# Kernel tuning notes

Hardware: AMD Instinct MI355X
Metric: run time of the kernel (lower is better)

## Reference

```python
import jax, jax.numpy as jnp
import numpy as np

B, S, D, H, K = 2, 2048, 1024, 16, 16


def setup_inputs() -> dict:
    key = jax.random.key(0)
    ks = jax.random.split(key, 8)
    s = 0.02
    def w(k, shape):
        return s * jax.random.normal(k, shape, jnp.float32)
    return {
        "x": jax.random.normal(ks[0], (B, S, D), jnp.float32),
        "Wq": w(ks[1], (D, D)), "bq": jnp.zeros((D,), jnp.float32),
        "Wk": w(ks[2], (D, D)), "bk": jnp.zeros((D,), jnp.float32),
        "Wv": w(ks[3], (D, D)), "bv": jnp.zeros((D,), jnp.float32),
        "Wo": w(ks[4], (D, D)), "bo": jnp.zeros((D,), jnp.float32),
        "Ws1": w(ks[5], (D, D // 2)), "bs1": jnp.zeros((D // 2,), jnp.float32),
        "Ws2": w(ks[6], (D // 2, 1)), "bs2": jnp.zeros((1,), jnp.float32),
    }


def reference(x, Wq, bq, Wk, bk, Wv, bv, Wo, bo, Ws1, bs1, Ws2, bs2):
    Bx, Sx, Dx = x.shape
    Dh = Dx // H
    # QKV projections -> [B, H, S, Dh]
    q = (x @ Wq + bq).reshape(Bx, Sx, H, Dh).transpose(0, 2, 1, 3)
    k = (x @ Wk + bk).reshape(Bx, Sx, H, Dh).transpose(0, 2, 1, 3)
    v = (x @ Wv + bv).reshape(Bx, Sx, H, Dh).transpose(0, 2, 1, 3)
    scores = jnp.einsum('bhqd,bhkd->bhqk', q, k) / np.float32(np.sqrt(Dh))
    # Lightning-indexer importance: [B, S]; identical across heads, so compute once.
    imp = jax.nn.sigmoid(jax.nn.relu(x @ Ws1 + bs1) @ Ws2 + bs2)[..., 0]
    _, idx = jax.lax.top_k(imp, K)  # [B, K]
    sel = jnp.zeros((Bx, Sx), bool).at[jnp.arange(Bx)[:, None], idx].set(True)
    # sparse mask: position (i, j) kept if row i OR column j is a top-k token
    m2 = sel[:, :, None] | sel[:, None, :]  # [B, S, S]
    masked = jnp.where(m2[:, None, :, :], scores, -jnp.inf)
    w = jax.nn.softmax(masked, axis=-1)
    att = jnp.einsum('bhqk,bhkd->bhqd', w, v).transpose(0, 2, 1, 3).reshape(Bx, Sx, Dx)
    return att @ Wo + bo
```

## Files before the change

### kernel.cpp

```cpp
#include <hip/hip_runtime.h>
#include <math.h>

constexpr int Bb = 2, Ss = 2048, Dd = 1024, Hh = 16, Kk = 16;
constexpr float DELTA = 0.02f;

typedef __bf16 bf16x8 __attribute__((ext_vector_type(8)));
typedef __bf16 bf16x4 __attribute__((ext_vector_type(4)));
typedef float  f32x4  __attribute__((ext_vector_type(4)));

__device__ __forceinline__ void gld_lds16(const void* g, void* l) {
    __builtin_amdgcn_global_load_lds(
        (const __attribute__((address_space(1))) unsigned int*)g,
        (__attribute__((address_space(3))) unsigned int*)l, 16, 0, 0);
}

__global__ void __launch_bounds__(256) prep_kernel(
    const float* __restrict__ x, __bf16* __restrict__ xb,
    __bf16* __restrict__ xbT,
    float* __restrict__ imp, float* __restrict__ hbuf,
    float* __restrict__ qkvsel, int* __restrict__ ccount,
    const float* __restrict__ Ws1, __bf16* __restrict__ W1Th,
    const float* __restrict__ bv, const float* __restrict__ bo,
    float* __restrict__ Y, float* __restrict__ zbuf,
    float* __restrict__ obuf)
{
    __shared__ float tile[32][33];
    const int bid = blockIdx.x;
    const int t   = threadIdx.x;

    if (bid < 4096) {
        int i = bid * 256 + t;
        if (i < Bb * Ss) imp[i] = 0.f;
        if (i < Bb * 64 * 512) hbuf[i] = 0.f;
        if (i < 3 * 32 * 1024) qkvsel[i] = 0.f;
        if (i < 2 * 256 * 1024) Y[i] = 0.f;
        if (i < 2 * 16 * 1024) zbuf[i] = bv[i & 1023];
        if (i < 2 * 16 * 1024) obuf[i] = bo[i & 1023];
        if (i < Bb) ccount[i] = 0;
        float4 v = ((const float4*)x)[i];
        bf16x4 h = { (__bf16)v.x, (__bf16)v.y, (__bf16)v.z, (__bf16)v.w };
        ((bf16x4*)xb)[i] = h;
        return;
    }
    if (bid < 8192) {
        int tid = bid - 4096;
        int b   = tid >> 11;
        int rem = tid & 2047;
        int rt  = rem >> 5;
        int ct  = rem & 31;
        int tx = t & 31, ty = t >> 5;
        const float* xp = x + (size_t)b * Ss * Dd;
        #pragma unroll
        for (int i2 = 0; i2 < 32; i2 += 8)
            tile[ty + i2][tx] = xp[(size_t)(rt * 32 + ty + i2) * 1024 + ct * 32 + tx];
        __syncthreads();
        __bf16* xT = xbT + (size_t)b * Dd * Ss;
        #pragma unroll
        for (int i2 = 0; i2 < 32; i2 += 8)
            xT[(size_t)(ct * 32 + ty + i2) * 2048 + rt * 32 + tx] = (__bf16)tile[tx][ty + i2];
        return;
    }
    {
        int tid = bid - 8192;
        int n0 = (tid & 15) * 32;
        int k0 = (tid >> 4) * 32;
        int tx = t & 31, ty = t >> 5;
        #pragma unroll
        for (int i2 = 0; i2 < 32; i2 += 8)
            tile[ty + i2][tx] = Ws1[(size_t)(k0 + ty + i2) * 512 + n0 + tx];
        __syncthreads();
        #pragma unroll
        for (int i2 = 0; i2 < 32; i2 += 8)
            W1Th[(size_t)(n0 + ty + i2) * 1024 + k0 + tx] = (__bf16)tile[tx][ty + i2];
    }
}

__global__ void __launch_bounds__(256) gemm_ind(
    const __bf16* __restrict__ xb, const __bf16* __restrict__ W1Th,
    const float* __restrict__ bs1, const float* __restrict__ Ws2,
    float* __restrict__ imp)
{
    __shared__ __bf16 As[64 * 64];
    __shared__ __bf16 Bs[128 * 64];

    const int cb   = blockIdx.x;
    const int bm   = blockIdx.y * 64;
    const int t    = threadIdx.x;
    const int wave = t >> 6;
    const int lane = t & 63;
    const int wm   = (wave & 1) * 32;
    const int wn   = (wave >> 1) * 64;
    const int fr   = lane & 15;
    const int fq   = lane >> 4;
    const int K    = Dd;

    const __bf16* BT = W1Th + (size_t)cb * 128 * 1024;

    f32x4 acc[2][4] = {};

    for (int k0 = 0; k0 < K; k0 += 64) {
        #pragma unroll
        for (int l = 0; l < 2; ++l) {
            int c = l * 256 + t;
            int row = c >> 3, seg = (c & 7) ^ (row & 7);
            gld_lds16(xb + (size_t)(bm + row) * K + k0 + seg * 8,
                      As + (size_t)(l * 256 + wave * 64) * 8);
        }
        #pragma unroll
        for (int l = 0; l < 4; ++l) {
            int c = l * 256 + t;
            int row = c >> 3, seg = (c & 7) ^ (row & 7);
            gld_lds16(BT + (size_t)row * K + k0 + seg * 8,
                      Bs + (size_t)(l * 256 + wave * 64) * 8);
        }
        __syncthreads();
        #pragma unroll
        for (int s = 0; s < 2; ++s) {
            bf16x8 af[2], bf[4];
            #pragma unroll
            for (int i = 0; i < 2; ++i) {
                int row = wm + i * 16 + fr;
                af[i] = *(const bf16x8*)(As + row * 64 + (((s * 4 + fq) ^ (row & 7)) * 8));
            }
            #pragma unroll
            for (int j = 0; j < 4; ++j) {
                int row = wn + j * 16 + fr;
                bf[j] = *(const bf16x8*)(Bs + row * 64 + (((s * 4 + fq) ^ (row & 7)) * 8));
            }
            #pragma unroll
            for (int i = 0; i < 2; ++i)
                #pragma unroll
                for (int j = 0; j < 4; ++j)
                    acc[i][j] = __builtin_amdgcn_mfma_f32_16x16x32_bf16(af[i], bf[j], acc[i][j], 0, 0, 0);
        }
        __syncthreads();
    }

    const int cr = (lane >> 4) * 4;
    const int cc = lane & 15;
    float bb[4], w2[4];
    #pragma unroll
    for (int j = 0; j < 4; ++j) {
        int col = cb * 128 + wn + j * 16 + cc;
        bb[j] = bs1[col];
        w2[j] = Ws2[col];
    }
    #pragma unroll
    for (int i = 0; i < 2; ++i) {
        #pragma unroll
        for (int r = 0; r < 4; ++r) {
            float vsum = 0.f;
            #pragma unroll
            for (int j = 0; j < 4; ++j)
                vsum += fmaxf(acc[i][j][r] + bb[j], 0.f) * w2[j];
            #pragma unroll
            for (int off = 8; off > 0; off >>= 1)
                vsum += __shfl_xor(vsum, off, 16);
            if (cc == 0)
                atomicAdd(imp + (bm + wm + i * 16 + cr + r), vsum);
        }
    }
}

__global__ void __launch_bounds__(1024) topk_cand(
    const float* __restrict__ imp, int* __restrict__ cand_idx,
    int* __restrict__ ccount)
{
    int b = blockIdx.x;
    int t = threadIdx.x;
    int wave = t >> 6, lane = t & 63;
    __shared__ float vals[Ss];
    __shared__ float sv[16];
    __shared__ int   si[16];
    __shared__ float thr_s;
    __shared__ int   cnt_s;

    vals[t]        = imp[b * Ss + t];
    vals[t + 1024] = imp[b * Ss + t + 1024];
    __syncthreads();

    for (int it = 0; it < Kk; ++it) {
        float v0 = vals[t], v1 = vals[t + 1024];
        float best = v0; int bidx = t;
        if (v1 > best) { best = v1; bidx = t + 1024; }
        #pragma unroll
        for (int off = 32; off > 0; off >>= 1) {
            float ov = __shfl_xor(best, off, 64);
            int   oi = __shfl_xor(bidx, off, 64);
            if (ov > best || (ov == best && oi < bidx)) { best = ov; bidx = oi; }
        }
        if (lane == 0) { sv[wave] = best; si[wave] = bidx; }
        __syncthreads();
        if (t == 0) {
            float bv = sv[0]; int br = si[0];
            #pragma unroll
            for (int w = 1; w < 16; ++w)
                if (sv[w] > bv || (sv[w] == bv && si[w] < br)) { bv = sv[w]; br = si[w]; }
            cand_idx[b * 64 + it] = br;
            vals[br] = -1e30f;
            if (it == Kk - 1) { thr_s = bv - DELTA; cnt_s = Kk; }
        }
        __syncthreads();
    }

    float thr = thr_s;
    if (vals[t] > thr) {
        int p = atomicAdd(&cnt_s, 1);
        if (p < 64) cand_idx[b * 64 + p] = t;
    }
    if (vals[t + 1024] > thr) {
        int p = atomicAdd(&cnt_s, 1);
        if (p < 64) cand_idx[b * 64 + p] = t + 1024;
    }
    __syncthreads();
    if (t == 0) ccount[b] = min(cnt_s, 64);
}

__global__ void __launch_bounds__(256) rescore_h(
    const float* __restrict__ x, const float* __restrict__ Ws1,
    const int* __restrict__ cand_idx, const int* __restrict__ ccount,
    float* __restrict__ hbuf)
{
    const int c = blockIdx.x, kc = blockIdx.y, b = blockIdx.z;
    if (c >= ccount[b]) return;
    const int row = cand_idx[b * 64 + c];
    const int t = threadIdx.x;
    const int k0 = kc * 64;

    __shared__ float xs[64];
    if (t < 16)
        ((float4*)xs)[t] = ((const float4*)(x + ((size_t)(b * Ss + row)) * Dd + k0))[t];
    __syncthreads();

    float a0 = 0.f, a1 = 0.f;
    const float* W = Ws1 + (size_t)k0 * 512;
    #pragma unroll 16
    for (int kk = 0; kk < 64; ++kk) {
        float xv = xs[kk];
        a0 = fmaf(xv, W[kk * 512 + t], a0);
        a1 = fmaf(xv, W[kk * 512 + t + 256], a1);
    }
    float* hb = hbuf + ((size_t)(b * 64 + c)) * 512;
    atomicAdd(hb + t, a0);
    atomicAdd(hb + t + 256, a1);
}

__global__ void __launch_bounds__(256) rescore_fin(
    const float* __restrict__ hbuf, const float* __restrict__ bs1,
    const float* __restrict__ Ws2, const int* __restrict__ ccount,
    float* __restrict__ candz)
{
    const int c = blockIdx.x, b = blockIdx.y;
    if (c >= ccount[b]) return;
    const int t = threadIdx.x;
    __shared__ float red[256];
    const float* hb = hbuf + ((size_t)(b * 64 + c)) * 512;
    float zp = fmaxf(hb[t] + bs1[t], 0.f) * Ws2[t]
             + fmaxf(hb[t + 256] + bs1[t + 256], 0.f) * Ws2[t + 256];
    red[t] = zp;
    __syncthreads();
    for (int off = 128; off > 0; off >>= 1) {
        if (t < off) red[t] += red[t + off];
        __syncthreads();
    }
    if (t == 0) candz[b * 64 + c] = red[0];
}

__global__ void __launch_bounds__(64) select_k(
    const float* __restrict__ candz, const int* __restrict__ cand_idx,
    const int* __restrict__ ccount, int* __restrict__ sel_idx)
{
    const int b = blockIdx.x, t = threadIdx.x;
    const int cnt = ccount[b];
    float val = (t < cnt) ? candz[b * 64 + t] : -1e30f;
    int   row = (t < cnt) ? cand_idx[b * 64 + t] : 0x7fffffff;

    for (int it = 0; it < Kk; ++it) {
        float bv = val; int br = row;
        #pragma unroll
        for (int off = 1; off < 64; off <<= 1) {
            float ov = __shfl_xor(bv, off, 64);
            int   orw = __shfl_xor(br, off, 64);
            if (ov > bv || (ov == bv && orw < br)) { bv = ov; br = orw; }
        }
        if (row == br) val = -1e30f;
        if (t == 0) sel_idx[b * Kk + it] = br;
    }
}

__global__ void __launch_bounds__(256) proj_sel(
    const float* __restrict__ x,
    const float* __restrict__ Wq, const float* __restrict__ Wk,
    const float* __restrict__ Wv,
    const int* __restrict__ sel_idx, float* __restrict__ qkvsel)
{
    const int cx = blockIdx.x;
    const int m  = blockIdx.y;
    const int kc = blockIdx.z;
    const int t  = threadIdx.x;
    __shared__ int   sj[32];
    __shared__ float xs[32][128];

    if (t < 32) sj[t] = sel_idx[t];
    __syncthreads();

    const int k0 = kc * 128;
    #pragma unroll
    for (int l = 0; l < 4; ++l) {
        int c = l * 256 + t;
        int r = c >> 5, kq = c & 31;
        int b = r >> 4;
        float4 v = *(const float4*)(x + ((size_t)(b * Ss + sj[r])) * Dd + k0 + kq * 4);
        *(float4*)&xs[r][kq * 4] = v;
    }
    __syncthreads();

    const float* W = (m == 0) ? Wq : (m == 1) ? Wk : Wv;
    const int col = cx * 128 + (t & 127);
    const int rh  = t >> 7;
    float acc[16] = {};
    #pragma unroll 4
    for (int kk = 0; kk < 128; ++kk) {
        float wv = W[(size_t)(k0 + kk) * 1024 + col];
        #pragma unroll
        for (int r = 0; r < 16; ++r)
            acc[r] = fmaf(xs[rh * 16 + r][kk], wv, acc[r]);
    }
    #pragma unroll
    for (int r = 0; r < 16; ++r)
        atomicAdd(qkvsel + (size_t)(m * 32 + rh * 16 + r) * 1024 + col, acc[r]);
}

__global__ void __launch_bounds__(256) build_cdvo(
    const float* __restrict__ Wq, const float* __restrict__ Wk,
    const float* __restrict__ Wo,
    const float* __restrict__ bq, const float* __restrict__ bk,
    const float* __restrict__ bv,
    const float* __restrict__ qkvsel, float* __restrict__ beta,
    __bf16* __restrict__ ET, __bf16* __restrict__ VoT)
{
    const int nx = blockIdx.x;
    const int h  = blockIdx.y;
    const int b  = blockIdx.z;
    const int t  = threadIdx.x;
    __shared__ float qs[16][64], ks[16][64], vs[16][64];
    __shared__ float wt[128][65];

    #pragma unroll
    for (int l = 0; l < 12; ++l) {
        int c = l * 256 + t;
        int mat = c >> 10, rem = c & 1023;
        int row = rem >> 6, d = rem & 63;
        const float* bias = (mat == 0) ? bq : (mat == 1) ? bk : bv;
        float v = qkvsel[(size_t)(mat * 32 + b * 16 + row) * 1024 + h * 64 + d]
                + bias[h * 64 + d];
        if (mat == 0) qs[row][d] = v;
        else if (mat == 1) ks[row][d] = v;
        else vs[row][d] = v;
    }
    __syncthreads();

    if (nx == 0 && t < 16) {
        float a = 0.f;
        #pragma unroll 8
        for (int d = 0; d < 64; ++d) a = fmaf(bq[h * 64 + d], ks[t][d], a);
        beta[b * 256 + h * 16 + t] = a;
    }

    const int nl = t & 127;
    const int n  = nx * 128 + nl;
    const int sg = t >> 7;

    #pragma unroll
    for (int l = 0; l < 8; ++l) {
        int c = l * 256 + t;
        int rn = c >> 4, c4 = c & 15;
        float4 v = *(const float4*)(Wq + (size_t)(nx * 128 + rn) * 1024 + h * 64 + c4 * 4);
        wt[rn][c4 * 4 + 0] = v.x; wt[rn][c4 * 4 + 1] = v.y;
        wt[rn][c4 * 4 + 2] = v.z; wt[rn][c4 * 4 + 3] = v.w;
    }
    __syncthreads();
    {
        float acc[8] = {};
        #pragma unroll 8
        for (int d = 0; d < 64; ++d) {
            float wv = wt[nl][d];
            #pragma unroll
            for (int s = 0; s < 8; ++s)
                acc[s] = fmaf(wv, ks[sg * 8 + s][d], acc[s]);
        }
        #pragma unroll
        for (int s = 0; s < 8; ++s)
            ET[(size_t)(b * 512 + h * 16 + sg * 8 + s) * 1024 + n] = (__bf16)acc[s];
    }
    __syncthreads();

    #pragma unroll
    for (int l = 0; l < 8; ++l) {
        int c = l * 256 + t;
        int rn = c >> 4, c4 = c & 15;
        float4 v = *(const float4*)(Wk + (size_t)(nx * 128 + rn) * 1024 + h * 64 + c4 * 4);
        wt[rn][c4 * 4 + 0] = v.x; wt[rn][c4 * 4 + 1] = v.y;
        wt[rn][c4 * 4 + 2] = v.z; wt[rn][c4 * 4 + 3] = v.w;
    }
    __syncthreads();
    {
        float acc[8] = {};
        #pragma unroll 8
        for (int d = 0; d < 64; ++d) {
            float wv = wt[nl][d];
            #pragma unroll
            for (int s = 0; s < 8; ++s)
                acc[s] = fmaf(wv, qs[sg * 8 + s][d], acc[s]);
        }
        #pragma unroll
        for (int s = 0; s < 8; ++s)
            ET[(size_t)(b * 512 + 256 + h * 16 + sg * 8 + s) * 1024 + n] = (__bf16)acc[s];
    }

    {
        float acc[8] = {};
        #pragma unroll 8
        for (int d = 0; d < 64; ++d) {
            float wv = Wo[(size_t)(h * 64 + d) * 1024 + n];
            #pragma unroll
            for (int s = 0; s < 8; ++s)
                acc[s] = fmaf(wv, vs[sg * 8 + s][d], acc[s]);
        }
        #pragma unroll
        for (int s = 0; s < 8; ++s)
            VoT[((size_t)b * 1024 + n) * 256 + h * 16 + sg * 8 + s] = (__bf16)acc[s];
    }
}

__global__ void __launch_bounds__(256) gemm_scores(
    const __bf16* __restrict__ xb, const __bf16* __restrict__ ET,
    float* __restrict__ Ssp, float* __restrict__ SdT)
{
    __shared__ __bf16 As[64 * 64];
    __shared__ __bf16 Bs[128 * 64];

    const int b    = blockIdx.z;
    const int bn   = blockIdx.x * 128;
    const int bm   = blockIdx.y * 64;
    const int t    = threadIdx.x;
    const int wave = t >> 6;
    const int lane = t & 63;
    const int wm   = (wave & 1) * 32;
    const int wn   = (wave >> 1) * 64;
    const int fr   = lane & 15;
    const int fq   = lane >> 4;
    const int K    = Dd;

    const __bf16* A  = xb + (size_t)b * Ss * Dd;
    const __bf16* BT = ET + (size_t)b * 512 * 1024 + (size_t)bn * 1024;

    f32x4 acc[2][4] = {};

    for (int k0 = 0; k0 < K; k0 += 64) {
        #pragma unroll
        for (int l = 0; l < 2; ++l) {
            int c = l * 256 + t;
            int row = c >> 3, seg = (c & 7) ^ (row & 7);
            gld_lds16(A + (size_t)(bm + row) * K + k0 + seg * 8,
                      As + (size_t)(l * 256 + wave * 64) * 8);
        }
        #pragma unroll
        for (int l = 0; l < 4; ++l) {
            int c = l * 256 + t;
            int row = c >> 3, seg = (c & 7) ^ (row & 7);
            gld_lds16(BT + (size_t)row * K + k0 + seg * 8,
                      Bs + (size_t)(l * 256 + wave * 64) * 8);
        }
        __syncthreads();
        #pragma unroll
        for (int s = 0; s < 2; ++s) {
            bf16x8 af[2], bf[4];
            #pragma unroll
            for (int i = 0; i < 2; ++i) {
                int row = wm + i * 16 + fr;
                af[i] = *(const bf16x8*)(As + row * 64 + (((s * 4 + fq) ^ (row & 7)) * 8));
            }
            #pragma unroll
            for (int j = 0; j < 4; ++j) {
                int row = wn + j * 16 + fr;
                bf[j] = *(const bf16x8*)(Bs + row * 64 + (((s * 4 + fq) ^ (row & 7)) * 8));
            }
            #pragma unroll
            for (int i = 0; i < 2; ++i)
                #pragma unroll
                for (int j = 0; j < 4; ++j)
                    acc[i][j] = __builtin_amdgcn_mfma_f32_16x16x32_bf16(af[i], bf[j], acc[i][j], 0, 0, 0);
        }
        __syncthreads();
    }

    const int cr = (lane >> 4) * 4;
    const int cc = lane & 15;
    #pragma unroll
    for (int j = 0; j < 4; ++j) {
        int col = bn + wn + j * 16 + cc;
        #pragma unroll
        for (int i = 0; i < 2; ++i) {
            int row0 = bm + wm + i * 16 + cr;
            if (col < 256) {
                #pragma unroll
                for (int r = 0; r < 4; ++r)
                    Ssp[((size_t)b * 2048 + row0 + r) * 256 + col] = acc[i][j][r];
            } else {
                *(f32x4*)(SdT + ((size_t)b * 256 + col - 256) * 2048 + row0) = acc[i][j];
            }
        }
    }
}

__global__ void __launch_bounds__(256) sm_sparse(
    const float* __restrict__ Ssp, const float* __restrict__ beta,
    __bf16* __restrict__ Wsp)
{
    const int b = blockIdx.y;
    const int r = blockIdx.x * 4 + (threadIdx.x >> 6);
    const int l = threadIdx.x & 63;
    float4 v  = *(const float4*)(Ssp + ((size_t)b * 2048 + r) * 256 + l * 4);
    float4 bt = *(const float4*)(beta + b * 256 + l * 4);
    float e0 = __expf((v.x + bt.x) * 0.125f);
    float e1 = __expf((v.y + bt.y) * 0.125f);
    float e2 = __expf((v.z + bt.z) * 0.125f);
    float e3 = __expf((v.w + bt.w) * 0.125f);
    float ps = e0 + e1 + e2 + e3;
    ps += __shfl_xor(ps, 1, 64);
    ps += __shfl_xor(ps, 2, 64);
    float inv = 1.f / ps;
    bf16x4 w = { (__bf16)(e0 * inv), (__bf16)(e1 * inv),
                 (__bf16)(e2 * inv), (__bf16)(e3 * inv) };
    *(bf16x4*)(Wsp + ((size_t)b * 2048 + r) * 256 + l * 4) = w;
}

__global__ void __launch_bounds__(256) sm_dense(
    const float* __restrict__ SdT, __bf16* __restrict__ WdT)
{
    const int b = blockIdx.y, cx = blockIdx.x;
    const int t = threadIdx.x;
    __shared__ float red[256];
    const float* Sp = SdT + ((size_t)b * 256 + cx) * 2048;
    float4 v0 = *(const float4*)(Sp + t * 8);
    float4 v1 = *(const float4*)(Sp + t * 8 + 4);
    float e[8];
    e[0] = __expf(v0.x * 0.125f); e[1] = __expf(v0.y * 0.125f);
    e[2] = __expf(v0.z * 0.125f); e[3] = __expf(v0.w * 0.125f);
    e[4] = __expf(v1.x * 0.125f); e[5] = __expf(v1.y * 0.125f);
    e[6] = __expf(v1.z * 0.125f); e[7] = __expf(v1.w * 0.125f);
    float ps = 0.f;
    #pragma unroll
    for (int i = 0; i < 8; ++i) ps += e[i];
    red[t] = ps;
    __syncthreads();
    for (int off = 128; off > 0; off >>= 1) {
        if (t < off) red[t] += red[t + off];
        __syncthreads();
    }
    float inv = 1.f / red[0];
    bf16x8 w;
    #pragma unroll
    for (int i = 0; i < 8; ++i) w[i] = (__bf16)(e[i] * inv);
    *(bf16x8*)(WdT + ((size_t)b * 256 + cx) * 2048 + t * 8) = w;
}

__global__ void __launch_bounds__(256) gemm_bt(
    const __bf16* __restrict__ A0, const __bf16* __restrict__ BT0,
    const float* __restrict__ bias, float* __restrict__ C0,
    int N, int K, size_t sA, size_t sB, size_t sC, int kchunks)
{
    __shared__ __bf16 As[64 * 64];
    __shared__ __bf16 Bs[128 * 64];

    const int batch = blockIdx.z / kchunks;
    const int kc    = blockIdx.z % kchunks;
    const __bf16* A  = A0 + (size_t)batch * sA;
    const __bf16* BT = BT0 + (size_t)batch * sB;
    float* C = C0 + (size_t)batch * sC;

    const int t    = threadIdx.x;
    const int wave = t >> 6;
    const int lane = t & 63;
    const int bm   = blockIdx.y * 64;
    const int bn   = blockIdx.x * 128;
    const int wm   = (wave & 1) * 32;
    const int wn   = (wave >> 1) * 64;
    const int fr   = lane & 15;
    const int fq   = lane >> 4;
    const int KC   = K / kchunks;
    const int kend = (kc + 1) * KC;

    f32x4 acc[2][4] = {};

    for (int k0 = kc * KC; k0 < kend; k0 += 64) {
        #pragma unroll
        for (int l = 0; l < 2; ++l) {
            int c = l * 256 + t;
            int row = c >> 3, seg = (c & 7) ^ (row & 7);
            gld_lds16(A + (size_t)(bm + row) * K + k0 + seg * 8,
                      As + (size_t)(l * 256 + wave * 64) * 8);
        }
        #pragma unroll
        for (int l = 0; l < 4; ++l) {
            int c = l * 256 + t;
            int row = c >> 3, seg = (c & 7) ^ (row & 7);
            gld_lds16(BT + (size_t)(bn + row) * K + k0 + seg * 8,
                      Bs + (size_t)(l * 256 + wave * 64) * 8);
        }
        __syncthreads();
        #pragma unroll
        for (int s = 0; s < 2; ++s) {
            bf16x8 af[2], bf[4];
            #pragma unroll
            for (int i = 0; i < 2; ++i) {
                int row = wm + i * 16 + fr;
                af[i] = *(const bf16x8*)(As + row * 64 + (((s * 4 + fq) ^ (row & 7)) * 8));
            }
            #pragma unroll
            for (int j = 0; j < 4; ++j) {
                int row = wn + j * 16 + fr;
                bf[j] = *(const bf16x8*)(Bs + row * 64 + (((s * 4 + fq) ^ (row & 7)) * 8));
            }
            #pragma unroll
            for (int i = 0; i < 2; ++i)
                #pragma unroll
                for (int j = 0; j < 4; ++j)
                    acc[i][j] = __builtin_amdgcn_mfma_f32_16x16x32_bf16(af[i], bf[j], acc[i][j], 0, 0, 0);
        }
        __syncthreads();
    }

    const int cr = (lane >> 4) * 4;
    const int cc = lane & 15;
    #pragma unroll
    for (int j = 0; j < 4; ++j) {
        int col = bn + wn + j * 16 + cc;
        if (kchunks == 1) {
            float bb = bias ? bias[col] : 0.f;
            #pragma unroll
            for (int i = 0; i < 2; ++i)
                #pragma unroll
                for (int r = 0; r < 4; ++r)
                    C[(size_t)(bm + wm + i * 16 + cr + r) * N + col] = acc[i][j][r] + bb;
        } else {
            #pragma unroll
            for (int i = 0; i < 2; ++i)
                #pragma unroll
                for (int r = 0; r < 4; ++r)
                    atomicAdd(C + (size_t)(bm + wm + i * 16 + cr + r) * N + col, acc[i][j][r]);
        }
    }
}

__global__ void __launch_bounds__(256) dense_z2(
    const float* __restrict__ Y, const float* __restrict__ Wv,
    float* __restrict__ zbuf)
{
    const int h = blockIdx.x, kc = blockIdx.y, b = blockIdx.z;
    const int t = threadIdx.x;
    __shared__ float Ys[16][128];
    const int k0 = kc * 128;
    #pragma unroll
    for (int l = 0; l < 2; ++l) {
        int c = l * 256 + t;
        int row = c >> 5, c4 = c & 31;
        *(float4*)&Ys[row][c4 * 4] =
            *(const float4*)(Y + ((size_t)(b * 256 + h * 16 + row)) * 1024 + k0 + c4 * 4);
    }
    __syncthreads();
    const int d = t & 63, tg = t >> 6;
    float acc[4] = {};
    #pragma unroll 8
    for (int kk = 0; kk < 128; ++kk) {
        float wv = Wv[(size_t)(k0 + kk) * 1024 + h * 64 + d];
        #pragma unroll
        for (int tt = 0; tt < 4; ++tt)
            acc[tt] = fmaf(Ys[tg * 4 + tt][kk], wv, acc[tt]);
    }
    #pragma unroll
    for (int tt = 0; tt < 4; ++tt)
        atomicAdd(zbuf + ((size_t)(b * 16 + tg * 4 + tt)) * 1024 + h * 64 + d, acc[tt]);
}

__global__ void __launch_bounds__(256) dense_out2(
    const float* __restrict__ zbuf, const float* __restrict__ Wo,
    float* __restrict__ obuf)
{
    const int nt = blockIdx.x, kc = blockIdx.y, b = blockIdx.z;
    const int t = threadIdx.x;
    __shared__ float zs[16][128];
    const int k0 = kc * 128;
    #pragma unroll
    for (int l = 0; l < 2; ++l) {
        int c = l * 256 + t;
        int row = c >> 5, c4 = c & 31;
        *(float4*)&zs[row][c4 * 4] =
            *(const float4*)(zbuf + ((size_t)(b * 16 + row)) * 1024 + k0 + c4 * 4);
    }
    __syncthreads();
    const int n = nt * 64 + (t & 63), tg = t >> 6;
    float acc[4] = {};
    #pragma unroll 8
    for (int kk = 0; kk < 128; ++kk) {
        float wv = Wo[(size_t)(k0 + kk) * 1024 + n];
        #pragma unroll
        for (int tt = 0; tt < 4; ++tt)
            acc[tt] = fmaf(zs[tg * 4 + tt][kk], wv, acc[tt]);
    }
    #pragma unroll
    for (int tt = 0; tt < 4; ++tt)
        atomicAdd(obuf + ((size_t)(b * 16 + tg * 4 + tt)) * 1024 + n, acc[tt]);
}

__global__ void __launch_bounds__(256) scatter_out(
    const float* __restrict__ obuf, const int* __restrict__ sel_idx,
    float* __restrict__ out)
{
    const int bid = blockIdx.x;
    const int b = bid >> 4, row = bid & 15;
    const int i = sel_idx[b * 16 + row];
    f32x4 v = *(const f32x4*)(obuf + ((size_t)(b * 16 + row)) * 1024 + threadIdx.x * 4);
    *(f32x4*)(out + ((size_t)(b * 2048 + i)) * 1024 + threadIdx.x * 4) = v;
}

extern "C" void kernel_launch(void* const* d_in, const int* in_sizes, int n_in,
                              void* d_out, int out_size, void* d_ws, size_t ws_size,
                              hipStream_t stream)
{
    const float* x   = (const float*)d_in[0];
    const float* Wq  = (const float*)d_in[1];
    const float* bq  = (const float*)d_in[2];
    const float* Wk  = (const float*)d_in[3];
    const float* bk  = (const float*)d_in[4];
    const float* Wv  = (const float*)d_in[5];
    const float* bv  = (const float*)d_in[6];
    const float* Wo  = (const float*)d_in[7];
    const float* bo  = (const float*)d_in[8];
    const float* Ws1 = (const float*)d_in[9];
    const float* bs1 = (const float*)d_in[10];
    const float* Ws2 = (const float*)d_in[11];
    float* out = (float*)d_out;

    const size_t MSD = (size_t)Bb * Ss * Dd;

    char* p = (char*)d_ws;
    __bf16* xb    = (__bf16*)p; p += MSD * sizeof(__bf16);
    __bf16* xbT   = (__bf16*)p; p += MSD * sizeof(__bf16);
    __bf16* W1Th  = (__bf16*)p; p += (size_t)512 * 1024 * sizeof(__bf16);
    __bf16* ET    = (__bf16*)p; p += (size_t)2 * 512 * 1024 * sizeof(__bf16);
    __bf16* VoT   = (__bf16*)p; p += (size_t)2 * 1024 * 256 * sizeof(__bf16);
    __bf16* Wsp   = (__bf16*)p; p += (size_t)2 * 2048 * 256 * sizeof(__bf16);
    __bf16* WdT   = (__bf16*)p; p += (size_t)2 * 256 * 2048 * sizeof(__bf16);
    float* Ssp    = (float*)p; p += (size_t)2 * 2048 * 256 * sizeof(float);
    float* SdT    = (float*)p; p += (size_t)2 * 256 * 2048 * sizeof(float);
    float* Y      = (float*)p; p += (size_t)2 * 256 * 1024 * sizeof(float);
    float* zbuf   = (float*)p; p += (size_t)2 * 16 * 1024 * sizeof(float);
    float* obuf   = (float*)p; p += (size_t)2 * 16 * 1024 * sizeof(float);
    float* imp    = (float*)p; p += (size_t)Bb * Ss * sizeof(float);
    float* hbuf   = (float*)p; p += (size_t)Bb * 64 * 512 * sizeof(float);
    float* qkvsel = (float*)p; p += (size_t)3 * 32 * 1024 * sizeof(float);
    float* beta   = (float*)p; p += (size_t)2 * 256 * sizeof(float);
    float* candz  = (float*)p; p += (size_t)Bb * 64 * sizeof(float);
    int* sel_idx  = (int*)p; p += (size_t)Bb * Kk * sizeof(int);
    int* cand_idx = (int*)p; p += (size_t)Bb * 64 * sizeof(int);
    int* ccount   = (int*)p; p += Bb * sizeof(int);

    prep_kernel<<<dim3(8704), 256, 0, stream>>>(
        x, xb, xbT, imp, hbuf, qkvsel, ccount, Ws1, W1Th,
        bv, bo, Y, zbuf, obuf);
    gemm_ind<<<dim3(4, 64), 256, 0, stream>>>(xb, W1Th, bs1, Ws2, imp);
    topk_cand<<<dim3(Bb), 1024, 0, stream>>>(imp, cand_idx, ccount);
    rescore_h<<<dim3(64, 16, Bb), 256, 0, stream>>>(x, Ws1, cand_idx, ccount, hbuf);
    rescore_fin<<<dim3(64, Bb), 256, 0, stream>>>(hbuf, bs1, Ws2, ccount, candz);
    select_k<<<dim3(Bb), 64, 0, stream>>>(candz, cand_idx, ccount, sel_idx);
    proj_sel<<<dim3(8, 3, 8), 256, 0, stream>>>(x, Wq, Wk, Wv, sel_idx, qkvsel);
    build_cdvo<<<dim3(8, 16, 2), 256, 0, stream>>>(
        Wq, Wk, Wo, bq, bk, bv, qkvsel, beta, ET, VoT);
    gemm_scores<<<dim3(4, 32, 2), 256, 0, stream>>>(xb, ET, Ssp, SdT);
    sm_sparse<<<dim3(512, 2), 256, 0, stream>>>(Ssp, beta, Wsp);
    sm_dense<<<dim3(256, 2), 256, 0, stream>>>(SdT, WdT);
    gemm_bt<<<dim3(8, 32, 2), 256, 0, stream>>>(
        Wsp, VoT, bo, out, 1024, 256,
        (size_t)2048 * 256, (size_t)1024 * 256, (size_t)2048 * 1024, 1);
    gemm_bt<<<dim3(8, 4, 4), 256, 0, stream>>>(
        WdT, xbT, nullptr, Y, 1024, 2048,
        (size_t)256 * 2048, (size_t)1024 * 2048, (size_t)256 * 1024, 2);
    dense_z2<<<dim3(16, 8, 2), 256, 0, stream>>>(Y, Wv, zbuf);
    dense_out2<<<dim3(16, 8, 2), 256, 0, stream>>>(zbuf, Wo, obuf);
    scatter_out<<<dim3(32), 256, 0, stream>>>(obuf, sel_idx, out);
}
```

Baseline: 277.1 us.

## Fuse small kernels via last-block-done counters and merged launches

Several tiny serial kernels are folded into their producers using an atomic counter so the last finishing block runs the follow-on step: top-k candidate selection into the indexer GEMM, rescore finalization and select into rescore, and scatter into the final dense kernel. The sparse and dense softmaxes are merged into one launch, and the two gemm_bt calls become a single grid. The aim is to cut kernel launch overhead and the gaps between dependent kernels. In exchange, top-k now runs on a single 256-thread block instead of 1024 threads, and it relies on threadfence-based cross-block synchronization.

```diff
diff --git a/kernel.cpp b/kernel.cpp
--- a/kernel.cpp
+++ b/kernel.cpp
@@ -22,7 +22,7 @@
     const float* __restrict__ Ws1, __bf16* __restrict__ W1Th,
     const float* __restrict__ bv, const float* __restrict__ bo,
     float* __restrict__ Y, float* __restrict__ zbuf,
-    float* __restrict__ obuf)
+    float* __restrict__ obuf, int* __restrict__ cnt)
 {
     __shared__ float tile[32][33];
     const int bid = blockIdx.x;
@@ -37,6 +37,7 @@
         if (i < 2 * 16 * 1024) zbuf[i] = bv[i & 1023];
         if (i < 2 * 16 * 1024) obuf[i] = bo[i & 1023];
         if (i < Bb) ccount[i] = 0;
+        if (i < 8) cnt[i] = 0;
         float4 v = ((const float4*)x)[i];
         bf16x4 h = { (__bf16)v.x, (__bf16)v.y, (__bf16)v.z, (__bf16)v.w };
         ((bf16x4*)xb)[i] = h;
@@ -75,13 +76,20 @@
     }
 }
 
-__global__ void __launch_bounds__(256) gemm_ind(
+__global__ void __launch_bounds__(256) gemm_ind_topk(
     const __bf16* __restrict__ xb, const __bf16* __restrict__ W1Th,
     const float* __restrict__ bs1, const float* __restrict__ Ws2,
-    float* __restrict__ imp)
+    float* __restrict__ imp, int* __restrict__ cnt,
+    int* __restrict__ cand_idx, int* __restrict__ ccount)
 {
     __shared__ __bf16 As[64 * 64];
     __shared__ __bf16 Bs[128 * 64];
+    __shared__ float vals[2048];
+    __shared__ float sv[4];
+    __shared__ int   si[4];
+    __shared__ float thr_s;
+    __shared__ int   cnt_s;
+    __shared__ int   lastf;
 
     const int cb   = blockIdx.x;
     const int bm   = blockIdx.y * 64;
@@ -160,29 +168,26 @@
                 atomicAdd(imp + (bm + wm + i * 16 + cr + r), vsum);
         }
     }
-}
-
-__global__ void __launch_bounds__(1024) topk_cand(
-    const float* __restrict__ imp, int* __restrict__ cand_idx,
-    int* __restrict__ ccount)
-{
-    int b = blockIdx.x;
-    int t = threadIdx.x;
-    int wave = t >> 6, lane = t & 63;
-    __shared__ float vals[Ss];
-    __shared__ float sv[16];
-    __shared__ int   si[16];
-    __shared__ float thr_s;
-    __shared__ int   cnt_s;
-
-    vals[t]        = imp[b * Ss + t];
-    vals[t + 1024] = imp[b * Ss + t + 1024];
+
+    __threadfence();
+    const int bq = blockIdx.y >> 5;
+    if (t == 0) lastf = (atomicAdd(&cnt[bq], 1) == 127);
+    __syncthreads();
+    if (!lastf) return;
+    __threadfence();
+
+    #pragma unroll
+    for (int e = 0; e < 8; ++e)
+        vals[t + 256 * e] = imp[bq * Ss + t + 256 * e];
     __syncthreads();
 
     for (int it = 0; it < Kk; ++it) {
-        float v0 = vals[t], v1 = vals[t + 1024];
-        float best = v0; int bidx = t;
-        if (v1 > best) { best = v1; bidx = t + 1024; }
+        float best = vals[t]; int bidx = t;
+        #pragma unroll
+        for (int e = 1; e < 8; ++e) {
+            float v = vals[t + 256 * e];
+            if (v > best) { best = v; bidx = t + 256 * e; }
+        }
         #pragma unroll
         for (int off = 32; off > 0; off >>= 1) {
             float ov = __shfl_xor(best, off, 64);
@@ -194,9 +199,9 @@
         if (t == 0) {
             float bv = sv[0]; int br = si[0];
             #pragma unroll
-            for (int w = 1; w < 16; ++w)
+            for (int w = 1; w < 4; ++w)
                 if (sv[w] > bv || (sv[w] == bv && si[w] < br)) { bv = sv[w]; br = si[w]; }
-            cand_idx[b * 64 + it] = br;
+            cand_idx[bq * 64 + it] = br;
             vals[br] = -1e30f;
             if (it == Kk - 1) { thr_s = bv - DELTA; cnt_s = Kk; }
         }
@@ -204,87 +209,85 @@
     }
 
     float thr = thr_s;
-    if (vals[t] > thr) {
-        int p = atomicAdd(&cnt_s, 1);
-        if (p < 64) cand_idx[b * 64 + p] = t;
-    }
-    if (vals[t + 1024] > thr) {
-        int p = atomicAdd(&cnt_s, 1);
-        if (p < 64) cand_idx[b * 64 + p] = t + 1024;
-    }
-    __syncthreads();
-    if (t == 0) ccount[b] = min(cnt_s, 64);
-}
-
-__global__ void __launch_bounds__(256) rescore_h(
+    #pragma unroll
+    for (int e = 0; e < 8; ++e) {
+        if (vals[t + 256 * e] > thr) {
+            int p = atomicAdd(&cnt_s, 1);
+            if (p < 64) cand_idx[bq * 64 + p] = t + 256 * e;
+        }
+    }
+    __syncthreads();
+    if (t == 0) ccount[bq] = min(cnt_s, 64);
+}
+
+__global__ void __launch_bounds__(256) rescore_all(
     const float* __restrict__ x, const float* __restrict__ Ws1,
     const int* __restrict__ cand_idx, const int* __restrict__ ccount,
-    float* __restrict__ hbuf)
+    float* __restrict__ hbuf, const float* __restrict__ bs1,
+    const float* __restrict__ Ws2, int* __restrict__ cnt,
+    int* __restrict__ sel_idx)
 {
     const int c = blockIdx.x, kc = blockIdx.y, b = blockIdx.z;
-    if (c >= ccount[b]) return;
-    const int row = cand_idx[b * 64 + c];
     const int t = threadIdx.x;
-    const int k0 = kc * 64;
-
     __shared__ float xs[64];
-    if (t < 16)
-        ((float4*)xs)[t] = ((const float4*)(x + ((size_t)(b * Ss + row)) * Dd + k0))[t];
-    __syncthreads();
-
-    float a0 = 0.f, a1 = 0.f;
-    const float* W = Ws1 + (size_t)k0 * 512;
-    #pragma unroll 16
-    for (int kk = 0; kk < 64; ++kk) {
-        float xv = xs[kk];
-        a0 = fmaf(xv, W[kk * 512 + t], a0);
-        a1 = fmaf(xv, W[kk * 512 + t + 256], a1);
-    }
-    float* hb = hbuf + ((size_t)(b * 64 + c)) * 512;
-    atomicAdd(hb + t, a0);
-    atomicAdd(hb + t + 256, a1);
-}
-
-__global__ void __launch_bounds__(256) rescore_fin(
-    const float* __restrict__ hbuf, const float* __restrict__ bs1,
-    const float* __restrict__ Ws2, const int* __restrict__ ccount,
-    float* __restrict__ candz)
-{
-    const int c = blockIdx.x, b = blockIdx.y;
-    if (c >= ccount[b]) return;
-    const int t = threadIdx.x;
-    __shared__ float red[256];
-    const float* hb = hbuf + ((size_t)(b * 64 + c)) * 512;
-    float zp = fmaxf(hb[t] + bs1[t], 0.f) * Ws2[t]
-             + fmaxf(hb[t + 256] + bs1[t + 256], 0.f) * Ws2[t + 256];
-    red[t] = zp;
-    __syncthreads();
-    for (int off = 128; off > 0; off >>= 1) {
-        if (t < off) red[t] += red[t + off];
-        __syncthreads();
-    }
-    if (t == 0) candz[b * 64 + c] = red[0];
-}
-
-__global__ void __launch_bounds__(64) select_k(
-    const float* __restrict__ candz, const int* __restrict__ cand_idx,
-    const int* __restrict__ ccount, int* __restrict__ sel_idx)
-{
-    const int b = blockIdx.x, t = threadIdx.x;
-    const int cnt = ccount[b];
-    float val = (t < cnt) ? candz[b * 64 + t] : -1e30f;
-    int   row = (t < cnt) ? cand_idx[b * 64 + t] : 0x7fffffff;
-
-    for (int it = 0; it < Kk; ++it) {
-        float bv = val; int br = row;
-        #pragma unroll
-        for (int off = 1; off < 64; off <<= 1) {
-            float ov = __shfl_xor(bv, off, 64);
-            int   orw = __shfl_xor(br, off, 64);
-            if (ov > bv || (ov == bv && orw < br)) { bv = ov; br = orw; }
-        }
-        if (row == br) val = -1e30f;
-        if (t == 0) sel_idx[b * Kk + it] = br;
+    __shared__ int   lastf;
+    __shared__ float czv[64];
+    __shared__ int   cidx[64];
+
+    const int cntb = ccount[b];
+    if (c < cntb) {
+        const int row = cand_idx[b * 64 + c];
+        const int k0 = kc * 64;
+        if (t < 16)
+            ((float4*)xs)[t] = ((const float4*)(x + ((size_t)(b * Ss + row)) * Dd + k0))[t];
+        __syncthreads();
+
+        float a0 = 0.f, a1 = 0.f;
+        const float* W = Ws1 + (size_t)k0 * 512;
+        #pragma unroll 16
+        for (int kk = 0; kk < 64; ++kk) {
+            float xv = xs[kk];
+            a0 = fmaf(xv, W[kk * 512 + t], a0);
+            a1 = fmaf(xv, W[kk * 512 + t + 256], a1);
+        }
+        float* hb = hbuf + ((size_t)(b * 64 + c)) * 512;
+        atomicAdd(hb + t, a0);
+        atomicAdd(hb + t + 256, a1);
+    }
+
+    __threadfence();
+    if (t == 0) lastf = (atomicAdd(&cnt[2 + b], 1) == 1023);
+    __syncthreads();
+    if (!lastf) return;
+    __threadfence();
+
+    {
+        const int cc = t >> 2, part = t & 3;
+        const float* hb = hbuf + ((size_t)(b * 64 + cc)) * 512;
+        float z = 0.f;
+        const int j0 = part * 128;
+        for (int j = j0; j < j0 + 128; ++j)
+            z += fmaxf(hb[j] + bs1[j], 0.f) * Ws2[j];
+        z += __shfl_xor(z, 1, 4);
+        z += __shfl_xor(z, 2, 4);
+        if (part == 0) { czv[cc] = z; cidx[cc] = cand_idx[b * 64 + cc]; }
+    }
+    __syncthreads();
+
+    if (t < 64) {
+        float val = (t < cntb) ? czv[t] : -1e30f;
+        int   row = (t < cntb) ? cidx[t] : 0x7fffffff;
+        for (int it = 0; it < Kk; ++it) {
+            float bv = val; int br = row;
+            #pragma unroll
+            for (int off = 1; off < 64; off <<= 1) {
+                float ov = __shfl_xor(bv, off, 64);
+                int   orw = __shfl_xor(br, off, 64);
+                if (ov > bv || (ov == bv && orw < br)) { bv = ov; br = orw; }
+            }
+            if (row == br) val = -1e30f;
+            if (t == 0) sel_idx[b * Kk + it] = br;
+        }
     }
 }
 
@@ -514,77 +517,66 @@
     }
 }
 
-__global__ void __launch_bounds__(256) sm_sparse(
+__global__ void __launch_bounds__(256) sm_all(
     const float* __restrict__ Ssp, const float* __restrict__ beta,
-    __bf16* __restrict__ Wsp)
-{
+    __bf16* __restrict__ Wsp,
+    const float* __restrict__ SdT, __bf16* __restrict__ WdT)
+{
+    __shared__ float red[256];
     const int b = blockIdx.y;
-    const int r = blockIdx.x * 4 + (threadIdx.x >> 6);
-    const int l = threadIdx.x & 63;
-    float4 v  = *(const float4*)(Ssp + ((size_t)b * 2048 + r) * 256 + l * 4);
-    float4 bt = *(const float4*)(beta + b * 256 + l * 4);
-    float e0 = __expf((v.x + bt.x) * 0.125f);
-    float e1 = __expf((v.y + bt.y) * 0.125f);
-    float e2 = __expf((v.z + bt.z) * 0.125f);
-    float e3 = __expf((v.w + bt.w) * 0.125f);
-    float ps = e0 + e1 + e2 + e3;
-    ps += __shfl_xor(ps, 1, 64);
-    ps += __shfl_xor(ps, 2, 64);
-    float inv = 1.f / ps;
-    bf16x4 w = { (__bf16)(e0 * inv), (__bf16)(e1 * inv),
-                 (__bf16)(e2 * inv), (__bf16)(e3 * inv) };
-    *(bf16x4*)(Wsp + ((size_t)b * 2048 + r) * 256 + l * 4) = w;
-}
-
-__global__ void __launch_bounds__(256) sm_dense(
-    const float* __restrict__ SdT, __bf16* __restrict__ WdT)
-{
-    const int b = blockIdx.y, cx = blockIdx.x;
     const int t = threadIdx.x;
-    __shared__ float red[256];
-    const float* Sp = SdT + ((size_t)b * 256 + cx) * 2048;
-    float4 v0 = *(const float4*)(Sp + t * 8);
-    float4 v1 = *(const float4*)(Sp + t * 8 + 4);
-    float e[8];
-    e[0] = __expf(v0.x * 0.125f); e[1] = __expf(v0.y * 0.125f);
-    e[2] = __expf(v0.z * 0.125f); e[3] = __expf(v0.w * 0.125f);
-    e[4] = __expf(v1.x * 0.125f); e[5] = __expf(v1.y * 0.125f);
-    e[6] = __expf(v1.z * 0.125f); e[7] = __expf(v1.w * 0.125f);
-    float ps = 0.f;
-    #pragma unroll
-    for (int i = 0; i < 8; ++i) ps += e[i];
-    red[t] = ps;
-    __syncthreads();
-    for (int off = 128; off > 0; off >>= 1) {
-        if (t < off) red[t] += red[t + off];
-        __syncthreads();
-    }
-    float inv = 1.f / red[0];
-    bf16x8 w;
-    #pragma unroll
-    for (int i = 0; i < 8; ++i) w[i] = (__bf16)(e[i] * inv);
-    *(bf16x8*)(WdT + ((size_t)b * 256 + cx) * 2048 + t * 8) = w;
-}
-
-__global__ void __launch_bounds__(256) gemm_bt(
-    const __bf16* __restrict__ A0, const __bf16* __restrict__ BT0,
-    const float* __restrict__ bias, float* __restrict__ C0,
-    int N, int K, size_t sA, size_t sB, size_t sC, int kchunks)
-{
-    __shared__ __bf16 As[64 * 64];
-    __shared__ __bf16 Bs[128 * 64];
-
-    const int batch = blockIdx.z / kchunks;
-    const int kc    = blockIdx.z % kchunks;
-    const __bf16* A  = A0 + (size_t)batch * sA;
-    const __bf16* BT = BT0 + (size_t)batch * sB;
-    float* C = C0 + (size_t)batch * sC;
-
-    const int t    = threadIdx.x;
+
+    if (blockIdx.x < 512) {
+        const int r = blockIdx.x * 4 + (t >> 6);
+        const int l = t & 63;
+        float4 v  = *(const float4*)(Ssp + ((size_t)b * 2048 + r) * 256 + l * 4);
+        float4 bt = *(const float4*)(beta + b * 256 + l * 4);
+        float e0 = __expf((v.x + bt.x) * 0.125f);
+        float e1 = __expf((v.y + bt.y) * 0.125f);
+        float e2 = __expf((v.z + bt.z) * 0.125f);
+        float e3 = __expf((v.w + bt.w) * 0.125f);
+        float ps = e0 + e1 + e2 + e3;
+        ps += __shfl_xor(ps, 1, 64);
+        ps += __shfl_xor(ps, 2, 64);
+        float inv = 1.f / ps;
+        bf16x4 w = { (__bf16)(e0 * inv), (__bf16)(e1 * inv),
+                     (__bf16)(e2 * inv), (__bf16)(e3 * inv) };
+        *(bf16x4*)(Wsp + ((size_t)b * 2048 + r) * 256 + l * 4) = w;
+    } else {
+        const int cx = blockIdx.x - 512;
+        const float* Sp = SdT + ((size_t)b * 256 + cx) * 2048;
+        float4 v0 = *(const float4*)(Sp + t * 8);
+        float4 v1 = *(const float4*)(Sp + t * 8 + 4);
+        float e[8];
+        e[0] = __expf(v0.x * 0.125f); e[1] = __expf(v0.y * 0.125f);
+        e[2] = __expf(v0.z * 0.125f); e[3] = __expf(v0.w * 0.125f);
+        e[4] = __expf(v1.x * 0.125f); e[5] = __expf(v1.y * 0.125f);
+        e[6] = __expf(v1.z * 0.125f); e[7] = __expf(v1.w * 0.125f);
+        float ps = 0.f;
+        #pragma unroll
+        for (int i = 0; i < 8; ++i) ps += e[i];
+        red[t] = ps;
+        __syncthreads();
+        for (int off = 128; off > 0; off >>= 1) {
+            if (t < off) red[t] += red[t + off];
+            __syncthreads();
+        }
+        float inv = 1.f / red[0];
+        bf16x8 w;
+        #pragma unroll
+        for (int i = 0; i < 8; ++i) w[i] = (__bf16)(e[i] * inv);
+        *(bf16x8*)(WdT + ((size_t)b * 256 + cx) * 2048 + t * 8) = w;
+    }
+}
+
+__device__ __forceinline__ void gemm_bt_body(
+    __bf16* As, __bf16* Bs,
+    const __bf16* __restrict__ A, const __bf16* __restrict__ BT,
+    const float* __restrict__ bias, float* __restrict__ C,
+    int N, int K, int bm, int bn, int kc, int kchunks, int t)
+{
     const int wave = t >> 6;
     const int lane = t & 63;
-    const int bm   = blockIdx.y * 64;
-    const int bn   = blockIdx.x * 128;
     const int wm   = (wave & 1) * 32;
     const int wn   = (wave >> 1) * 64;
     const int fr   = lane & 15;
@@ -654,6 +646,33 @@
     }
 }
 
+__global__ void __launch_bounds__(256) gemm_bt2x(
+    const __bf16* __restrict__ Wsp, const __bf16* __restrict__ VoT,
+    const float* __restrict__ bo, float* __restrict__ out,
+    const __bf16* __restrict__ WdT, const __bf16* __restrict__ xbT,
+    float* __restrict__ Y)
+{
+    __shared__ __bf16 As[64 * 64];
+    __shared__ __bf16 Bs[128 * 64];
+    const int t = threadIdx.x;
+    int id = blockIdx.x;
+    if (id < 512) {
+        int bx = id & 7, by = (id >> 3) & 31, bz = id >> 8;
+        gemm_bt_body(As, Bs,
+                     Wsp + (size_t)bz * 2048 * 256, VoT + (size_t)bz * 1024 * 256,
+                     bo, out + (size_t)bz * 2048 * 1024,
+                     1024, 256, by * 64, bx * 128, 0, 1, t);
+    } else {
+        id -= 512;
+        int bx = id & 7, by = (id >> 3) & 3, z = id >> 5;
+        int batch = z >> 1, kc = z & 1;
+        gemm_bt_body(As, Bs,
+                     WdT + (size_t)batch * 256 * 2048, xbT + (size_t)batch * 1024 * 2048,
+                     nullptr, Y + (size_t)batch * 256 * 1024,
+                     1024, 2048, by * 64, bx * 128, kc, 2, t);
+    }
+}
+
 __global__ void __launch_bounds__(256) dense_z2(
     const float* __restrict__ Y, const float* __restrict__ Wv,
     float* __restrict__ zbuf)
@@ -684,13 +703,16 @@
         atomicAdd(zbuf + ((size_t)(b * 16 + tg * 4 + tt)) * 1024 + h * 64 + d, acc[tt]);
 }
 
-__global__ void __launch_bounds__(256) dense_out2(
+__global__ void __launch_bounds__(256) dense_fin(
     const float* __restrict__ zbuf, const float* __restrict__ Wo,
-    float* __restrict__ obuf)
+    float* __restrict__ obuf, int* __restrict__ cnt,
+    const int* __restrict__ sel_idx, float* __restrict__ out)
 {
     const int nt = blockIdx.x, kc = blockIdx.y, b = blockIdx.z;
     const int t = threadIdx.x;
     __shared__ float zs[16][128];
+    __shared__ int lastf;
+    __shared__ int sj[16];
     const int k0 = kc * 128;
     #pragma unroll
     for (int l = 0; l < 2; ++l) {
@@ -712,17 +734,19 @@
     #pragma unroll
     for (int tt = 0; tt < 4; ++tt)
         atomicAdd(obuf + ((size_t)(b * 16 + tg * 4 + tt)) * 1024 + n, acc[tt]);
-}
-
-__global__ void __launch_bounds__(256) scatter_out(
-    const float* __restrict__ obuf, const int* __restrict__ sel_idx,
-    float* __restrict__ out)
-{
-    const int bid = blockIdx.x;
-    const int b = bid >> 4, row = bid & 15;
-    const int i = sel_idx[b * 16 + row];
-    f32x4 v = *(const f32x4*)(obuf + ((size_t)(b * 16 + row)) * 1024 + threadIdx.x * 4);
-    *(f32x4*)(out + ((size_t)(b * 2048 + i)) * 1024 + threadIdx.x * 4) = v;
+
+    __threadfence();
+    if (t == 0) lastf = (atomicAdd(&cnt[4 + b], 1) == 127);
+    __syncthreads();
+    if (!lastf) return;
+    __threadfence();
+    if (t < 16) sj[t] = sel_idx[b * 16 + t];
+    __syncthreads();
+    #pragma unroll
+    for (int r = 0; r < 16; ++r) {
+        float4 v = *(const float4*)(obuf + ((size_t)(b * 16 + r)) * 1024 + t * 4);
+        *(float4*)(out + ((size_t)(b * 2048 + sj[r])) * 1024 + t * 4) = v;
+    }
 }
 
 extern "C" void kernel_launch(void* const* d_in, const int* in_sizes, int n_in,
@@ -762,32 +786,24 @@
     float* hbuf   = (float*)p; p += (size_t)Bb * 64 * 512 * sizeof(float);
     float* qkvsel = (float*)p; p += (size_t)3 * 32 * 1024 * sizeof(float);
     float* beta   = (float*)p; p += (size_t)2 * 256 * sizeof(float);
-    float* candz  = (float*)p; p += (size_t)Bb * 64 * sizeof(float);
+    int* cnt      = (int*)p; p += 8 * sizeof(int);
     int* sel_idx  = (int*)p; p += (size_t)Bb * Kk * sizeof(int);
     int* cand_idx = (int*)p; p += (size_t)Bb * 64 * sizeof(int);
     int* ccount   = (int*)p; p += Bb * sizeof(int);
 
     prep_kernel<<<dim3(8704), 256, 0, stream>>>(
         x, xb, xbT, imp, hbuf, qkvsel, ccount, Ws1, W1Th,
-        bv, bo, Y, zbuf, obuf);
-    gemm_ind<<<dim3(4, 64), 256, 0, stream>>>(xb, W1Th, bs1, Ws2, imp);
-    topk_cand<<<dim3(Bb), 1024, 0, stream>>>(imp, cand_idx, ccount);
-    rescore_h<<<dim3(64, 16, Bb), 256, 0, stream>>>(x, Ws1, cand_idx, ccount, hbuf);
-    rescore_fin<<<dim3(64, Bb), 256, 0, stream>>>(hbuf, bs1, Ws2, ccount, candz);
-    select_k<<<dim3(Bb), 64, 0, stream>>>(candz, cand_idx, ccount, sel_idx);
+        bv, bo, Y, zbuf, obuf, cnt);
+    gemm_ind_topk<<<dim3(4, 64), 256, 0, stream>>>(
+        xb, W1Th, bs1, Ws2, imp, cnt, cand_idx, ccount);
+    rescore_all<<<dim3(64, 16, Bb), 256, 0, stream>>>(
+        x, Ws1, cand_idx, ccount, hbuf, bs1, Ws2, cnt, sel_idx);
     proj_sel<<<dim3(8, 3, 8), 256, 0, stream>>>(x, Wq, Wk, Wv, sel_idx, qkvsel);
     build_cdvo<<<dim3(8, 16, 2), 256, 0, stream>>>(
         Wq, Wk, Wo, bq, bk, bv, qkvsel, beta, ET, VoT);
     gemm_scores<<<dim3(4, 32, 2), 256, 0, stream>>>(xb, ET, Ssp, SdT);
-    sm_sparse<<<dim3(512, 2), 256, 0, stream>>>(Ssp, beta, Wsp);
-    sm_dense<<<dim3(256, 2), 256, 0, stream>>>(SdT, WdT);
-    gemm_bt<<<dim3(8, 32, 2), 256, 0, stream>>>(
-        Wsp, VoT, bo, out, 1024, 256,
-        (size_t)2048 * 256, (size_t)1024 * 256, (size_t)2048 * 1024, 1);
-    gemm_bt<<<dim3(8, 4, 4), 256, 0, stream>>>(
-        WdT, xbT, nullptr, Y, 1024, 2048,
-        (size_t)256 * 2048, (size_t)1024 * 2048, (size_t)256 * 1024, 2);
+    sm_all<<<dim3(768, 2), 256, 0, stream>>>(Ssp, beta, Wsp, SdT, WdT);
+    gemm_bt2x<<<dim3(640), 256, 0, stream>>>(Wsp, VoT, bo, out, WdT, xbT, Y);
     dense_z2<<<dim3(16, 8, 2), 256, 0, stream>>>(Y, Wv, zbuf);
-    dense_out2<<<dim3(16, 8, 2), 256, 0, stream>>>(zbuf, Wo, obuf);
-    scatter_out<<<dim3(32), 256, 0, stream>>>(obuf, sel_idx, out);
-}
+    dense_fin<<<dim3(16, 8, 2), 256, 0, stream>>>(zbuf, Wo, obuf, cnt, sel_idx, out);
+}
```

Result: slower. 439.3 us (+58.5%).
